# Performance work log

Hardware: AMD Instinct MI355X
Metric: run time of the kernel (lower is better)

## Reference

```python
import jax, jax.numpy as jnp
import numpy as np

EPS = 1e-06


def _conv1x1(x, W, b):
    # x: [B,C,H,W], W: [O,C], b: [O] -> [B,O,H,W]
    return jnp.einsum('oc,bchw->bohw', W, x) + b[None, :, None, None]


def _l2_norm(x):
    # normalize over channel dim (-2) per position, matching torch.norm(p=2, dim=-2)
    return x / jnp.linalg.norm(x, axis=-2, keepdims=True)


def setup_inputs() -> dict:
    key = jax.random.key(0)
    ks = jax.random.split(key, 8)
    B, C, H, W = 8, 512, 64, 64
    Cq = C // 8
    s = 0.02
    return {
        'x': jax.random.normal(ks[0], (B, C, H, W), jnp.float32),
        'Wq': jax.random.normal(ks[1], (Cq, C), jnp.float32) * s,
        'bq': jax.random.normal(ks[2], (Cq,), jnp.float32) * s,
        'Wk': jax.random.normal(ks[3], (Cq, C), jnp.float32) * s,
        'bk': jax.random.normal(ks[4], (Cq,), jnp.float32) * s,
        'Wv': jax.random.normal(ks[5], (C, C), jnp.float32) * s,
        'bv': jax.random.normal(ks[6], (C,), jnp.float32) * s,
        'gamma': jax.random.normal(ks[7], (1,), jnp.float32),
    }


def reference(x, Wq, bq, Wk, bk, Wv, bv, gamma):
    B, C, H, W = x.shape
    N = H * W
    Q = _conv1x1(x, Wq, bq).reshape(B, -1, N)   # [B,C',N]
    K = _conv1x1(x, Wk, bk).reshape(B, -1, N)   # [B,C',N]
    V = _conv1x1(x, Wv, bv).reshape(B, C, N)    # [B,C,N]

    Qn = _l2_norm(Q).transpose(0, 2, 1)         # [B,N,C']
    Kn = _l2_norm(K)                            # [B,C',N]

    # taylor denominator: 1 / (N + Q . (sum_n K + eps))
    tailor_sum = 1.0 / (N + jnp.einsum('bnc,bc->bn', Qn, Kn.sum(-1) + EPS))  # [B,N]

    value_sum = V.sum(-1)                        # [B,C]
    matrix = jnp.einsum('bmn,bcn->bmc', Kn, V)   # [B,C',C]
    matrix_sum = value_sum[:, :, None] + jnp.einsum('bnm,bmc->bcn', Qn, matrix)  # [B,C,N]

    weight_value = (matrix_sum * tailor_sum[:, None, :]).reshape(B, C, H, W)
    return gamma * weight_value
```

## Files before the change

### kernel.cpp

```cpp
#include <hip/hip_runtime.h>
#include <math.h>

#define B_   8
#define C_   512
#define CQ   64
#define N_   4096
#define EPSF 1e-6f
#define LS   40
#define LS2  72
#define LSX  520
#define LTS  264

typedef short  shortx8 __attribute__((ext_vector_type(8)));
typedef short  shortx4 __attribute__((ext_vector_type(4)));
typedef float  floatx4 __attribute__((ext_vector_type(4)));

__device__ __forceinline__ short f2bf(float f) {
    unsigned u = __builtin_bit_cast(unsigned, f);
    u += 0x7FFFu + ((u >> 16) & 1u);
    return (short)(u >> 16);
}
__device__ __forceinline__ float bf2f(short h) {
    unsigned u = ((unsigned)(unsigned short)h) << 16;
    return __builtin_bit_cast(float, u);
}
__device__ __forceinline__ shortx8 ldf8(const short* p) {
    return *(const shortx8*)p;
}

__global__ __launch_bounds__(256) void pcast(
    const float* __restrict__ Wq, const float* __restrict__ Wk,
    const float* __restrict__ Wv, short* __restrict__ Wqk, short* __restrict__ Wvb)
{
    int i = (blockIdx.x * 256 + threadIdx.x) * 4;
    float4 v; short* dst;
    if (i < 2 * CQ * C_) {
        const float* src = (i < CQ * C_) ? (Wq + i) : (Wk + i - CQ * C_);
        v = *(const float4*)src;
        dst = Wqk + i;
    } else {
        int j = i - 2 * CQ * C_;
        v = *(const float4*)(Wv + j);
        dst = Wvb + j;
    }
    const float* f = (const float*)&v;
    shortx4 o = { f2bf(f[0]), f2bf(f[1]), f2bf(f[2]), f2bf(f[3]) };
    *(shortx4*)dst = o;
}

__global__ __launch_bounds__(256, 2) void xprep(
    const float* __restrict__ x, short* __restrict__ xT)
{
    const int cht = blockIdx.x, nt2 = blockIdx.y, b = blockIdx.z;
    const int ch0 = cht * 256, n0 = nt2 * 128;
    const int tid = threadIdx.x;

    __shared__ __attribute__((aligned(16))) short T_l[128][LTS];

    const float* src = x + ((size_t)b * C_ + ch0 + tid) * N_ + n0;
#pragma unroll 8
    for (int i = 0; i < 32; i++) {
        float4 v = *(const float4*)(src + i * 4);
        const float* f = (const float*)&v;
#pragma unroll
        for (int j = 0; j < 4; j++)
            T_l[i * 4 + j][tid] = f2bf(f[j]);
    }
    __syncthreads();

    const int n = tid >> 1, h = tid & 1;
    short* dst = xT + ((size_t)b * N_ + n0 + n) * C_ + ch0 + h * 128;
#pragma unroll
    for (int i = 0; i < 16; i++)
        *(shortx8*)(dst + i * 8) = *(const shortx8*)&T_l[n][h * 128 + i * 8];
}

__global__ __launch_bounds__(256, 2) void k1_qk(
    const short* __restrict__ xT, const short* __restrict__ Wqk,
    const float* __restrict__ bq, const float* __restrict__ bk,
    short* __restrict__ Qnt, short* __restrict__ Kn, float* __restrict__ Ksum)
{
    const int b   = blockIdx.y;
    const int n0  = blockIdx.x * 64;
    const int tid = threadIdx.x;
    const int lane = tid & 63, wid = tid >> 6;
    const int waveM = wid >> 1, waveN = wid & 1;
    const int quad = lane >> 4, ln = lane & 15;

    __shared__ __attribute__((aligned(16))) short x_l[64][LSX];
    __shared__ float bias_l[128];

    if (tid < 128) bias_l[tid] = (tid < 64) ? bq[tid] : bk[tid - 64];

    {
        const int r = tid >> 2, off = (tid & 3) * 128;
        const short* srcT = xT + ((size_t)b * N_ + n0 + r) * C_ + off;
#pragma unroll
        for (int i = 0; i < 16; i++)
            *(shortx8*)&x_l[r][off + i * 8] = *(const shortx8*)(srcT + i * 8);
    }
    __syncthreads();

    const short* Ab = Wqk + (size_t)(waveM * 64 + ln) * C_ + quad * 8;
    const floatx4 z4 = {0.f, 0.f, 0.f, 0.f};
    floatx4 acc[4][2];
#pragma unroll
    for (int mt = 0; mt < 4; mt++) { acc[mt][0] = z4; acc[mt][1] = z4; }

#pragma unroll 4
    for (int kc = 0; kc < 16; ++kc) {
        shortx8 af[4];
#pragma unroll
        for (int mt = 0; mt < 4; mt++)
            af[mt] = ldf8(Ab + (size_t)mt * 16 * C_ + kc * 32);
#pragma unroll
        for (int nt = 0; nt < 2; nt++) {
            shortx8 bf8 = ldf8(&x_l[waveN * 32 + nt * 16 + ln][kc * 32 + quad * 8]);
#pragma unroll
            for (int mt = 0; mt < 4; mt++)
                acc[mt][nt] = __builtin_amdgcn_mfma_f32_16x16x32_bf16(af[mt], bf8, acc[mt][nt], 0, 0, 0);
        }
    }

#pragma unroll
    for (int mt = 0; mt < 4; mt++)
#pragma unroll
        for (int r = 0; r < 4; r++) {
            float bias = bias_l[waveM * 64 + mt * 16 + quad * 4 + r];
#pragma unroll
            for (int nt = 0; nt < 2; nt++) acc[mt][nt][r] += bias;
        }
#pragma unroll
    for (int nt = 0; nt < 2; nt++) {
        float s = 0.f;
#pragma unroll
        for (int mt = 0; mt < 4; mt++)
#pragma unroll
            for (int r = 0; r < 4; r++) s += acc[mt][nt][r] * acc[mt][nt][r];
        s += __shfl_xor(s, 16);
        s += __shfl_xor(s, 32);
        float inv = rsqrtf(s);
#pragma unroll
        for (int mt = 0; mt < 4; mt++)
#pragma unroll
            for (int r = 0; r < 4; r++) acc[mt][nt][r] *= inv;
    }

    if (waveM == 0) {
        short* Qb = Qnt + (size_t)b * N_ * CQ;
#pragma unroll
        for (int nt = 0; nt < 2; nt++) {
            int n = n0 + waveN * 32 + nt * 16 + ln;
#pragma unroll
            for (int mt = 0; mt < 4; mt++) {
                shortx4 v;
#pragma unroll
                for (int r = 0; r < 4; r++) v[r] = f2bf(acc[mt][nt][r]);
                *(shortx4*)(Qb + (size_t)n * CQ + mt * 16 + quad * 4) = v;
            }
        }
    } else {
        short* Kb = Kn + (size_t)b * CQ * N_;
#pragma unroll
        for (int mt = 0; mt < 4; mt++)
#pragma unroll
            for (int r = 0; r < 4; r++) {
                int m = mt * 16 + quad * 4 + r;
                float s = 0.f;
#pragma unroll
                for (int nt = 0; nt < 2; nt++) {
                    int n = n0 + waveN * 32 + nt * 16 + ln;
                    float v = acc[mt][nt][r];
                    Kb[(size_t)m * N_ + n] = f2bf(v);
                    s += v;
                }
                s += __shfl_xor(s, 1); s += __shfl_xor(s, 2);
                s += __shfl_xor(s, 4); s += __shfl_xor(s, 8);
                if (ln == 0) atomicAdd(&Ksum[b * CQ + m], s);
            }
    }
}

__global__ __launch_bounds__(256, 4) void k2_kx(
    const float* __restrict__ x, const short* __restrict__ Kn,
    float* __restrict__ KX, float* __restrict__ xsum)
{
    const int jt = blockIdx.x, ks = blockIdx.y, b = blockIdx.z;
    const int j0 = jt * 64, nbase = ks * 512;
    const int tid = threadIdx.x;
    const int lane = tid & 63, wid = tid >> 6;
    const int quad = lane >> 4, ln = lane & 15;

    const short* Ab = Kn + (size_t)b * CQ * N_ + (size_t)ln * N_ + nbase + quad * 8;
    const float* Bs = x + (size_t)b * C_ * N_
                    + (size_t)(j0 + wid * 16 + ln) * N_ + nbase + quad * 8;

    const floatx4 z4 = {0.f, 0.f, 0.f, 0.f};
    floatx4 acc[4] = {z4, z4, z4, z4};
    float xsacc = 0.f;

#pragma unroll 4
    for (int kc = 0; kc < 16; ++kc) {
        float4 u0 = *(const float4*)(Bs + kc * 32);
        float4 u1 = *(const float4*)(Bs + kc * 32 + 4);
        shortx8 af[4];
#pragma unroll
        for (int mt = 0; mt < 4; mt++)
            af[mt] = ldf8(Ab + (size_t)mt * 16 * N_ + kc * 32);
        const float* f0 = (const float*)&u0;
        const float* f1 = (const float*)&u1;
        shortx8 bf8;
#pragma unroll
        for (int q = 0; q < 4; q++) {
            bf8[q]     = f2bf(f0[q]); xsacc += f0[q];
            bf8[q + 4] = f2bf(f1[q]); xsacc += f1[q];
        }
#pragma unroll
        for (int mt = 0; mt < 4; mt++)
            acc[mt] = __builtin_amdgcn_mfma_f32_16x16x32_bf16(af[mt], bf8, acc[mt], 0, 0, 0);
    }

    xsacc += __shfl_xor(xsacc, 16);
    xsacc += __shfl_xor(xsacc, 32);
    if (quad == 0) atomicAdd(&xsum[b * C_ + j0 + wid * 16 + ln], xsacc);

    float* KXb = KX + (size_t)b * CQ * C_;
#pragma unroll
    for (int mt = 0; mt < 4; mt++)
#pragma unroll
        for (int r = 0; r < 4; r++) {
            int m = mt * 16 + quad * 4 + r;
            atomicAdd(&KXb[(size_t)m * C_ + j0 + wid * 16 + ln], acc[mt][r]);
        }
}

__global__ __launch_bounds__(256, 2) void k3_m(
    const float* __restrict__ KX, const short* __restrict__ Wvb,
    const float* __restrict__ bv, const float* __restrict__ Ksum,
    const float* __restrict__ xsum,
    short* __restrict__ Mt, float* __restrict__ vs)
{
    const int ct = blockIdx.x, b = blockIdx.y;
    const int c0 = ct * 64;
    const int tid = threadIdx.x;
    const int lane = tid & 63, wid = tid >> 6;
    const int quad = lane >> 4, ln = lane & 15;

    __shared__ short A_l[2][64][LS];
    __shared__ short B_l[2][64][LS];
    __shared__ float xsl[C_], Ksl[64], bvl[64], vsp[4][64];

    xsl[tid] = xsum[(size_t)b * C_ + tid];
    xsl[tid + 256] = xsum[(size_t)b * C_ + tid + 256];
    if (tid < 64) { Ksl[tid] = Ksum[b * CQ + tid]; bvl[tid] = bv[c0 + tid]; }

    const int rA = tid >> 2, oA = (tid & 3) * 8;
    const short* As = Wvb + (size_t)(c0 + rA) * C_ + oA;
    const float* Bs = KX + ((size_t)b * CQ + rA) * C_ + oA;

    shortx8 aC = *(const shortx8*)As;
    float4 b0 = *(const float4*)(Bs);
    float4 b1 = *(const float4*)(Bs + 4);

    auto stage = [&](int buf, shortx8 a, float4 q0, float4 q1) {
        *(shortx8*)&A_l[buf][rA][oA] = a;
        const float* f0 = (const float*)&q0;
        const float* f1 = (const float*)&q1;
        shortx8 t;
#pragma unroll
        for (int i = 0; i < 4; i++) { t[i] = f2bf(f0[i]); t[i + 4] = f2bf(f1[i]); }
        *(shortx8*)&B_l[buf][rA][oA] = t;
    };
    stage(0, aC, b0, b1);
    __syncthreads();

    const floatx4 z4 = {0.f, 0.f, 0.f, 0.f};
    floatx4 acc[4] = {z4, z4, z4, z4};
    float vsacc = 0.f;
    const int cv = tid & 63;

    int cur = 0;
    for (int it = 0; it < 16; ++it) {
        shortx8 aN; float4 n0v, n1v;
        if (it < 15) {
            const int off = (it + 1) * 32;
            aN  = *(const shortx8*)(As + off);
            n0v = *(const float4*)(Bs + off);
            n1v = *(const float4*)(Bs + off + 4);
        }
        shortx8 af[4];
#pragma unroll
        for (int ct2 = 0; ct2 < 4; ct2++)
            af[ct2] = ldf8(&A_l[cur][ct2 * 16 + ln][quad * 8]);
        shortx8 bf8 = ldf8(&B_l[cur][wid * 16 + ln][quad * 8]);
#pragma unroll
        for (int ct2 = 0; ct2 < 4; ct2++)
            acc[ct2] = __builtin_amdgcn_mfma_f32_16x16x32_bf16(af[ct2], bf8, acc[ct2], 0, 0, 0);
#pragma unroll
        for (int jj = 0; jj < 8; jj++)
            vsacc += bf2f(A_l[cur][cv][wid * 8 + jj]) * xsl[it * 32 + wid * 8 + jj];
        if (it < 15) stage(cur ^ 1, aN, n0v, n1v);
        __syncthreads();
        cur ^= 1;
    }

    vsp[wid][cv] = vsacc;
    __syncthreads();
    if (tid < 64)
        vs[(size_t)b * C_ + c0 + tid] =
            vsp[0][tid] + vsp[1][tid] + vsp[2][tid] + vsp[3][tid] + (float)N_ * bvl[tid];

    const int m = wid * 16 + ln;
    const float ksm = Ksl[m];
    short* Mb = Mt + (size_t)b * C_ * CQ;
#pragma unroll
    for (int ct2 = 0; ct2 < 4; ct2++)
#pragma unroll
        for (int r = 0; r < 4; r++) {
            int c = ct2 * 16 + quad * 4 + r;
            Mb[(size_t)(c0 + c) * CQ + m] = f2bf(acc[ct2][r] + ksm * bvl[c]);
        }
}

__global__ __launch_bounds__(256, 3) void k4_out(
    const short* __restrict__ Qnt, const short* __restrict__ Mt,
    const float* __restrict__ vs, const float* __restrict__ Ksum,
    const float* __restrict__ gamma, float* __restrict__ out)
{
    const int nt = blockIdx.x, ct = blockIdx.y, b = blockIdx.z;
    const int n0 = nt * 128, c0 = ct * 128;
    const int tid = threadIdx.x;
    const int lane = tid & 63, wid = tid >> 6;
    const int waveC = wid >> 1, waveN = wid & 1;
    const int quad = lane >> 4, ln = lane & 15;

    __shared__ short B_l[128][LS2];
    __shared__ float tsl[128], vsl[128], Ks_l[64];

    {
        int n = tid >> 1, h = tid & 1;
        const short* src = Qnt + ((size_t)b * N_ + n0 + n) * CQ + h * 32;
#pragma unroll
        for (int q = 0; q < 4; q++)
            *(shortx8*)&B_l[n][h * 32 + q * 8] = *(const shortx8*)(src + q * 8);
    }
    if (tid < 64)  Ks_l[tid] = Ksum[b * CQ + tid];
    if (tid < 128) vsl[tid]  = vs[(size_t)b * C_ + c0 + tid];
    __syncthreads();

    if (tid < 128) {
        const short* row = B_l[tid];
        float s = 0.f;
#pragma unroll
        for (int m = 0; m < 64; m++) s += bf2f(row[m]) * (Ks_l[m] + EPSF);
        tsl[tid] = 1.f / ((float)N_ + s);
    }
    __syncthreads();

    const floatx4 z4 = {0.f, 0.f, 0.f, 0.f};
    floatx4 acc[4][4];
#pragma unroll
    for (int i = 0; i < 4; i++)
#pragma unroll
        for (int j = 0; j < 4; j++) acc[i][j] = z4;

    const short* Am = Mt + (size_t)b * C_ * CQ
                    + (size_t)(c0 + waveC * 64 + ln) * CQ + quad * 8;
#pragma unroll
    for (int kc = 0; kc < 2; kc++) {
        shortx8 af[4];
#pragma unroll
        for (int ct2 = 0; ct2 < 4; ct2++)
            af[ct2] = ldf8(Am + (size_t)ct2 * 16 * CQ + kc * 32);
#pragma unroll
        for (int nt2 = 0; nt2 < 4; nt2++) {
            shortx8 bf8 = ldf8(&B_l[waveN * 64 + nt2 * 16 + ln][kc * 32 + quad * 8]);
#pragma unroll
            for (int ct2 = 0; ct2 < 4; ct2++)
                acc[ct2][nt2] = __builtin_amdgcn_mfma_f32_16x16x32_bf16(af[ct2], bf8, acc[ct2][nt2], 0, 0, 0);
        }
    }

    const float g = gamma[0];
    float* ob = out + (size_t)b * C_ * N_;
#pragma unroll
    for (int ct2 = 0; ct2 < 4; ct2++)
#pragma unroll
        for (int r = 0; r < 4; r++) {
            int cl = waveC * 64 + ct2 * 16 + quad * 4 + r;
            float vc = vsl[cl];
#pragma unroll
            for (int nt2 = 0; nt2 < 4; nt2++) {
                int nl = waveN * 64 + nt2 * 16 + ln;
                ob[(size_t)(c0 + cl) * N_ + n0 + nl] = g * tsl[nl] * (vc + acc[ct2][nt2][r]);
            }
        }
}

extern "C" void kernel_launch(void* const* d_in, const int* in_sizes, int n_in,
                              void* d_out, int out_size, void* d_ws, size_t ws_size,
                              hipStream_t stream)
{
    (void)in_sizes; (void)n_in; (void)out_size; (void)ws_size;
    const float* x     = (const float*)d_in[0];
    const float* Wq    = (const float*)d_in[1];
    const float* bq    = (const float*)d_in[2];
    const float* Wk    = (const float*)d_in[3];
    const float* bk    = (const float*)d_in[4];
    const float* Wv    = (const float*)d_in[5];
    const float* bv    = (const float*)d_in[6];
    const float* gamma = (const float*)d_in[7];
    float* out = (float*)d_out;

    short* Qnt = (short*)d_ws;
    short* Kn  = Qnt + (size_t)B_ * N_ * CQ;
    float* Ksum = (float*)(Kn + (size_t)B_ * CQ * N_);
    float* xsum = Ksum + B_ * CQ;
    float* KX   = xsum + B_ * C_;
    short* Mt   = (short*)(KX + (size_t)B_ * CQ * C_);
    float* vs   = (float*)(Mt + (size_t)B_ * C_ * CQ);
    short* Wqk  = (short*)(vs + B_ * C_);
    short* Wvb  = Wqk + 2 * CQ * C_;
    short* xT   = Wvb + (size_t)C_ * C_;

    size_t zbytes = (size_t)(B_ * CQ + B_ * C_ + B_ * CQ * C_) * 4;
    hipMemsetAsync(Ksum, 0, zbytes, stream);

    pcast <<<dim3(320),       256, 0, stream>>>(Wq, Wk, Wv, Wqk, Wvb);
    xprep <<<dim3(2, 32, 8),  256, 0, stream>>>(x, xT);
    k1_qk <<<dim3(64, 8),     256, 0, stream>>>(xT, Wqk, bq, bk, Qnt, Kn, Ksum);
    k2_kx <<<dim3(8, 8, 8),   256, 0, stream>>>(x, Kn, KX, xsum);
    k3_m  <<<dim3(8, 8),      256, 0, stream>>>(KX, Wvb, bv, Ksum, xsum, Mt, vs);
    k4_out<<<dim3(32, 4, 8),  256, 0, stream>>>(Qnt, Mt, vs, Ksum, gamma, out);
}
```

Before: 226.4 us.

## Fuse x transpose-cast into QK kernel and replace KX atomics with partials

Removes the separate xprep kernel that wrote a bf16 transposed copy of x. k1_qk now reads fp32 x directly, converts it to bf16 and writes it into an XOR-swizzled shared layout to avoid bank conflicts. This drops one kernel launch and one global round trip through xT. k2_kx now writes per-split partial KX tiles instead of float atomics, and k3_m sums the 8 partials while loading. The memset for KX is removed, at the cost of 8x more KX traffic read in k3.

```diff
diff --git a/kernel.cpp b/kernel.cpp
--- a/kernel.cpp
+++ b/kernel.cpp
@@ -9,10 +9,10 @@
 #define LS   40
 #define LS2  72
 #define LSX  520
-#define LTS  264
 
 typedef short  shortx8 __attribute__((ext_vector_type(8)));
 typedef short  shortx4 __attribute__((ext_vector_type(4)));
+typedef short  shortx2 __attribute__((ext_vector_type(2)));
 typedef float  floatx4 __attribute__((ext_vector_type(4)));
 
 __device__ __forceinline__ short f2bf(float f) {
@@ -48,35 +48,8 @@
     *(shortx4*)dst = o;
 }
 
-__global__ __launch_bounds__(256, 2) void xprep(
-    const float* __restrict__ x, short* __restrict__ xT)
-{
-    const int cht = blockIdx.x, nt2 = blockIdx.y, b = blockIdx.z;
-    const int ch0 = cht * 256, n0 = nt2 * 128;
-    const int tid = threadIdx.x;
-
-    __shared__ __attribute__((aligned(16))) short T_l[128][LTS];
-
-    const float* src = x + ((size_t)b * C_ + ch0 + tid) * N_ + n0;
-#pragma unroll 8
-    for (int i = 0; i < 32; i++) {
-        float4 v = *(const float4*)(src + i * 4);
-        const float* f = (const float*)&v;
-#pragma unroll
-        for (int j = 0; j < 4; j++)
-            T_l[i * 4 + j][tid] = f2bf(f[j]);
-    }
-    __syncthreads();
-
-    const int n = tid >> 1, h = tid & 1;
-    short* dst = xT + ((size_t)b * N_ + n0 + n) * C_ + ch0 + h * 128;
-#pragma unroll
-    for (int i = 0; i < 16; i++)
-        *(shortx8*)(dst + i * 8) = *(const shortx8*)&T_l[n][h * 128 + i * 8];
-}
-
 __global__ __launch_bounds__(256, 2) void k1_qk(
-    const short* __restrict__ xT, const short* __restrict__ Wqk,
+    const float* __restrict__ x, const short* __restrict__ Wqk,
     const float* __restrict__ bq, const float* __restrict__ bk,
     short* __restrict__ Qnt, short* __restrict__ Kn, float* __restrict__ Ksum)
 {
@@ -92,12 +65,24 @@
 
     if (tid < 128) bias_l[tid] = (tid < 64) ? bq[tid] : bk[tid - 64];
 
-    {
-        const int r = tid >> 2, off = (tid & 3) * 128;
-        const short* srcT = xT + ((size_t)b * N_ + n0 + r) * C_ + off;
-#pragma unroll
-        for (int i = 0; i < 16; i++)
-            *(shortx8*)&x_l[r][off + i * 8] = *(const shortx8*)(srcT + i * 8);
+    const int nq = tid & 15, kp = tid >> 4;
+    const float* xb = x + (size_t)b * C_ * N_;
+#pragma unroll 4
+    for (int i = 0; i < 16; i++) {
+        const int ch = kp * 2 + 32 * i;
+        const float* p = xb + (size_t)ch * N_ + n0 + nq * 4;
+        float4 r0 = *(const float4*)(p);
+        float4 r1 = *(const float4*)(p + N_);
+        const float* f0 = (const float*)&r0;
+        const float* f1 = (const float*)&r1;
+        const int slot = ch >> 3, sub = ch & 7;
+#pragma unroll
+        for (int j = 0; j < 4; j++) {
+            const int n = nq * 4 + j;
+            const int pcol = ((slot ^ ((n >> 2) & 7)) << 3) + sub;
+            shortx2 t = { f2bf(f0[j]), f2bf(f1[j]) };
+            *(shortx2*)&x_l[n][pcol] = t;
+        }
     }
     __syncthreads();
 
@@ -115,7 +100,9 @@
             af[mt] = ldf8(Ab + (size_t)mt * 16 * C_ + kc * 32);
 #pragma unroll
         for (int nt = 0; nt < 2; nt++) {
-            shortx8 bf8 = ldf8(&x_l[waveN * 32 + nt * 16 + ln][kc * 32 + quad * 8]);
+            const int row = waveN * 32 + nt * 16 + ln;
+            const int pslot = (kc * 4 + quad) ^ ((row >> 2) & 7);
+            shortx8 bf8 = ldf8(&x_l[row][pslot << 3]);
 #pragma unroll
             for (int mt = 0; mt < 4; mt++)
                 acc[mt][nt] = __builtin_amdgcn_mfma_f32_16x16x32_bf16(af[mt], bf8, acc[mt][nt], 0, 0, 0);
@@ -183,7 +170,7 @@
 
 __global__ __launch_bounds__(256, 4) void k2_kx(
     const float* __restrict__ x, const short* __restrict__ Kn,
-    float* __restrict__ KX, float* __restrict__ xsum)
+    float* __restrict__ KXp, float* __restrict__ xsum)
 {
     const int jt = blockIdx.x, ks = blockIdx.y, b = blockIdx.z;
     const int j0 = jt * 64, nbase = ks * 512;
@@ -224,18 +211,18 @@
     xsacc += __shfl_xor(xsacc, 32);
     if (quad == 0) atomicAdd(&xsum[b * C_ + j0 + wid * 16 + ln], xsacc);
 
-    float* KXb = KX + (size_t)b * CQ * C_;
+    float* KXb = KXp + ((size_t)b * 8 + ks) * CQ * C_;
 #pragma unroll
     for (int mt = 0; mt < 4; mt++)
 #pragma unroll
         for (int r = 0; r < 4; r++) {
             int m = mt * 16 + quad * 4 + r;
-            atomicAdd(&KXb[(size_t)m * C_ + j0 + wid * 16 + ln], acc[mt][r]);
+            KXb[(size_t)m * C_ + j0 + wid * 16 + ln] = acc[mt][r];
         }
 }
 
 __global__ __launch_bounds__(256, 2) void k3_m(
-    const float* __restrict__ KX, const short* __restrict__ Wvb,
+    const float* __restrict__ KXp, const short* __restrict__ Wvb,
     const float* __restrict__ bv, const float* __restrict__ Ksum,
     const float* __restrict__ xsum,
     short* __restrict__ Mt, float* __restrict__ vs)
@@ -256,11 +243,28 @@
 
     const int rA = tid >> 2, oA = (tid & 3) * 8;
     const short* As = Wvb + (size_t)(c0 + rA) * C_ + oA;
-    const float* Bs = KX + ((size_t)b * CQ + rA) * C_ + oA;
+    const float* Bs = KXp + ((size_t)b * 8 * CQ + rA) * C_ + oA;
+    const size_t PS = (size_t)CQ * C_;
+
+    auto loadB = [&](int off, float4& o0, float4& o1) {
+        float s0[4] = {0.f, 0.f, 0.f, 0.f}, s1[4] = {0.f, 0.f, 0.f, 0.f};
+#pragma unroll
+        for (int p = 0; p < 8; p++) {
+            const float* q = Bs + p * PS + off;
+            float4 u0 = *(const float4*)(q);
+            float4 u1 = *(const float4*)(q + 4);
+            const float* g0 = (const float*)&u0;
+            const float* g1 = (const float*)&u1;
+#pragma unroll
+            for (int e = 0; e < 4; e++) { s0[e] += g0[e]; s1[e] += g1[e]; }
+        }
+        o0 = make_float4(s0[0], s0[1], s0[2], s0[3]);
+        o1 = make_float4(s1[0], s1[1], s1[2], s1[3]);
+    };
 
     shortx8 aC = *(const shortx8*)As;
-    float4 b0 = *(const float4*)(Bs);
-    float4 b1 = *(const float4*)(Bs + 4);
+    float4 b0, b1;
+    loadB(0, b0, b1);
 
     auto stage = [&](int buf, shortx8 a, float4 q0, float4 q1) {
         *(shortx8*)&A_l[buf][rA][oA] = a;
@@ -284,9 +288,8 @@
         shortx8 aN; float4 n0v, n1v;
         if (it < 15) {
             const int off = (it + 1) * 32;
-            aN  = *(const shortx8*)(As + off);
-            n0v = *(const float4*)(Bs + off);
-            n1v = *(const float4*)(Bs + off + 4);
+            aN = *(const shortx8*)(As + off);
+            loadB(off, n0v, n1v);
         }
         shortx8 af[4];
 #pragma unroll
@@ -416,20 +419,18 @@
     short* Kn  = Qnt + (size_t)B_ * N_ * CQ;
     float* Ksum = (float*)(Kn + (size_t)B_ * CQ * N_);
     float* xsum = Ksum + B_ * CQ;
-    float* KX   = xsum + B_ * C_;
-    short* Mt   = (short*)(KX + (size_t)B_ * CQ * C_);
+    float* KXp  = xsum + B_ * C_;
+    short* Mt   = (short*)(KXp + (size_t)B_ * 8 * CQ * C_);
     float* vs   = (float*)(Mt + (size_t)B_ * C_ * CQ);
     short* Wqk  = (short*)(vs + B_ * C_);
     short* Wvb  = Wqk + 2 * CQ * C_;
-    short* xT   = Wvb + (size_t)C_ * C_;
-
-    size_t zbytes = (size_t)(B_ * CQ + B_ * C_ + B_ * CQ * C_) * 4;
+
+    size_t zbytes = (size_t)(B_ * CQ + B_ * C_) * 4;
     hipMemsetAsync(Ksum, 0, zbytes, stream);
 
-    pcast <<<dim3(320),       256, 0, stream>>>(Wq, Wk, Wv, Wqk, Wvb);
-    xprep <<<dim3(2, 32, 8),  256, 0, stream>>>(x, xT);
-    k1_qk <<<dim3(64, 8),     256, 0, stream>>>(xT, Wqk, bq, bk, Qnt, Kn, Ksum);
-    k2_kx <<<dim3(8, 8, 8),   256, 0, stream>>>(x, Kn, KX, xsum);
-    k3_m  <<<dim3(8, 8),      256, 0, stream>>>(KX, Wvb, bv, Ksum, xsum, Mt, vs);
-    k4_out<<<dim3(32, 4, 8),  256, 0, stream>>>(Qnt, Mt, vs, Ksum, gamma, out);
-}
+    pcast <<<dim3(320),      256, 0, stream>>>(Wq, Wk, Wv, Wqk, Wvb);
+    k1_qk <<<dim3(64, 8),    256, 0, stream>>>(x, Wqk, bq, bk, Qnt, Kn, Ksum);
+    k2_kx <<<dim3(8, 8, 8),  256, 0, stream>>>(x, Kn, KXp, xsum);
+    k3_m  <<<dim3(8, 8),     256, 0, stream>>>(KXp, Wvb, bv, Ksum, xsum, Mt, vs);
+    k4_out<<<dim3(32, 4, 8), 256, 0, stream>>>(Qnt, Mt, vs, Ksum, gamma, out);
+}
```

After: 223.9 us. Within noise of the previous version (-1.1%).
